# Kernel optimization log

Measured on AMD Instinct MI355X. Metric: run time of the kernel, lower is better.

The kernel has to match this reference:

```python
import jax, jax.numpy as jnp
import numpy as np

N0, N1, N2 = 200000, 100000, 50000
E0, E1 = 1600000, 800000
IN_F, H_F, N_CLS = 128, 256, 64


def sage_conv(h_src, src_idx, dst_idx, num_dst, W_self, W_neigh, b):
    # DGL SAGEConv with aggregator_type='mean':
    #   h_neigh = mean over in-neighbors of h_src
    #   out = h_dst @ W_self + h_neigh @ W_neigh + b
    h_dst = h_src[:num_dst]
    msgs = h_src[src_idx]                                   # [E, F] gather
    summed = jax.ops.segment_sum(msgs, dst_idx, num_segments=num_dst)
    deg = jax.ops.segment_sum(jnp.ones((src_idx.shape[0],), h_src.dtype),
                              dst_idx, num_segments=num_dst)
    h_neigh = summed / jnp.maximum(deg, 1.0)[:, None]       # mean, safe for deg=0
    return h_dst @ W_self + h_neigh @ W_neigh + b


def setup_inputs() -> dict:
    key = jax.random.key(0)
    ks = jax.random.split(key, 10)
    s1 = 1.0 / np.sqrt(IN_F)
    s2 = 1.0 / np.sqrt(H_F)
    return {
        "x": jax.random.normal(ks[0], (N0, IN_F), jnp.float32),
        "src0": jax.random.randint(ks[1], (E0,), 0, N0, jnp.int64 if jax.config.jax_enable_x64 else jnp.int32),
        "dst0": jnp.sort(jax.random.randint(ks[2], (E0,), 0, N1)),
        "src1": jax.random.randint(ks[3], (E1,), 0, N1),
        "dst1": jnp.sort(jax.random.randint(ks[4], (E1,), 0, N2)),
        "num_dst0": N1,
        "num_dst1": N2,
        "W_self1": jax.random.normal(ks[5], (IN_F, H_F), jnp.float32) * s1,
        "W_neigh1": jax.random.normal(ks[6], (IN_F, H_F), jnp.float32) * s1,
        "b1": jnp.zeros((H_F,), jnp.float32),
        "W_self2": jax.random.normal(ks[7], (H_F, N_CLS), jnp.float32) * s2,
        "W_neigh2": jax.random.normal(ks[8], (H_F, N_CLS), jnp.float32) * s2,
        "b2": jnp.zeros((N_CLS,), jnp.float32),
    }


def reference(x, src0, dst0, src1, dst1, num_dst0, num_dst1,
              W_self1, W_neigh1, b1, W_self2, W_neigh2, b2):
    h = sage_conv(x, src0, dst0, num_dst0, W_self1, W_neigh1, b1)   # [N1, H]
    h = jax.nn.relu(h)
    h = sage_conv(h, src1, dst1, num_dst1, W_self2, W_neigh2, b2)   # [N2, C]
    return h
```

## Files before the change

### kernel.cpp

```cpp
#include <hip/hip_runtime.h>

constexpr int cN0  = 200000;
constexpr int cN1  = 100000;
constexpr int cN2  = 50000;
constexpr int cE0  = 1600000;
constexpr int cE1  = 800000;
constexpr int cIN  = 128;
constexpr int cH   = 256;
constexpr int cCLS = 64;

constexpr float QSTEP = 6.0f / 127.0f;
constexpr float QINV  = 127.0f / 6.0f;

using bf16x8 = __attribute__((ext_vector_type(8))) short;
using f32x4  = __attribute__((ext_vector_type(4))) float;

__device__ __forceinline__ float bflo(unsigned int u) {
    union { unsigned int i; float f; } v; v.i = u << 16; return v.f;
}
__device__ __forceinline__ float bfhi(unsigned int u) {
    union { unsigned int i; float f; } v; v.i = u & 0xFFFF0000u; return v.f;
}
__device__ __forceinline__ unsigned int f2bf(float f) {
    union { float f; unsigned int i; } v; v.f = f;
    return (v.i + 0x7FFFu + ((v.i >> 16) & 1u)) >> 16;
}

constexpr int XBLK = (cN0 * cIN / 8) / 256;
constexpr int WCNT = cH * cH + 2 * cCLS * cH;
constexpr int WBLK = WCNT / 256;
constexpr int RCNT = (cN1 + 1) + (cN2 + 1);
constexpr int RBLK = (RCNT + 255) / 256;

__global__ __launch_bounds__(256) void prep(
        const float* __restrict__ x,
        const float* __restrict__ Ws1, const float* __restrict__ Wn1,
        const float* __restrict__ Wn2, const float* __restrict__ Ws2,
        const int* __restrict__ dst0, const int* __restrict__ dst1,
        unsigned short* __restrict__ xb, unsigned int* __restrict__ xq,
        unsigned short* __restrict__ Wt1, unsigned short* __restrict__ Wt2,
        int* __restrict__ row0, int* __restrict__ row1) {
    const int b = blockIdx.x, tid = threadIdx.x;
    if (b < XBLK) {
        const int i = b * 256 + tid;
        const float4* p = (const float4*)x + (size_t)i * 2;
        float4 a = p[0], c = p[1];
        uint4 o;
        o.x = f2bf(a.x) | (f2bf(a.y) << 16);
        o.y = f2bf(a.z) | (f2bf(a.w) << 16);
        o.z = f2bf(c.x) | (f2bf(c.y) << 16);
        o.w = f2bf(c.z) | (f2bf(c.w) << 16);
        ((uint4*)xb)[i] = o;
        auto q8 = [](float v) -> unsigned int {
            int q = __float2int_rn(v * QINV);
            q = q > 127 ? 127 : (q < -127 ? -127 : q);
            return (unsigned int)q & 255u;
        };
        uint2 d;
        d.x = q8(a.x) | (q8(a.y) << 8) | (q8(a.z) << 16) | (q8(a.w) << 24);
        d.y = q8(c.x) | (q8(c.y) << 8) | (q8(c.z) << 16) | (q8(c.w) << 24);
        ((uint2*)xq)[i] = d;
    } else if (b < XBLK + WBLK) {
        const int wi = (b - XBLK) * 256 + tid;
        if (wi < cH * cH) {
            int n = wi >> 8, k = wi & 255;
            float v = (k < cIN) ? Ws1[k * cH + n] : Wn1[(k - cIN) * cH + n];
            Wt1[n * cH + k] = (unsigned short)f2bf(v);
        } else {
            int j = wi - cH * cH; int n = j >> 8, k = j & 255;
            float v = (n < cCLS) ? Wn2[k * cCLS + n] : Ws2[k * cCLS + (n - cCLS)];
            Wt2[n * cH + k] = (unsigned short)f2bf(v);
        }
    } else {
        const int ti = (b - XBLK - WBLK) * 256 + tid;
        if (ti <= cN1) {
            int lo = 0, hi = cE0;
            while (lo < hi) { int mid = (lo + hi) >> 1; if (dst0[mid] < ti) lo = mid + 1; else hi = mid; }
            row0[ti] = lo;
        } else {
            int d = ti - (cN1 + 1);
            if (d <= cN2) {
                int lo = 0, hi = cE1;
                while (lo < hi) { int mid = (lo + hi) >> 1; if (dst1[mid] < d) lo = mid + 1; else hi = mid; }
                row1[d] = lo;
            }
        }
    }
}

__global__ __launch_bounds__(256) void agg_i8(
        const uint2* __restrict__ xq,
        const int* __restrict__ sidx,
        const int* __restrict__ rows,
        unsigned short* __restrict__ nb,
        int num_dst) {
    const int tid = threadIdx.x, lane = tid & 63;
    const int m = blockIdx.x * 4 + (tid >> 6);
    if (m >= num_dst) return;
    const int sub = lane >> 4, t = lane & 15;
    const int e0 = rows[m], e1 = rows[m + 1];

    int acc[8];
    #pragma unroll
    for (int j = 0; j < 8; ++j) acc[j] = 0;
    auto addq = [&](uint2 v) {
        #pragma unroll
        for (int d = 0; d < 2; ++d) {
            unsigned int w = (&v.x)[d];
            acc[d * 4 + 0] += (int)(signed char)(w);
            acc[d * 4 + 1] += (int)(signed char)(w >> 8);
            acc[d * 4 + 2] += (int)(signed char)(w >> 16);
            acc[d * 4 + 3] += (int)(signed char)(w >> 24);
        }
    };

    int base = e0;
    for (; base + 16 <= e1; base += 16) {
        int sA = sidx[base + sub];
        int sB = sidx[base + 4 + sub];
        int sC = sidx[base + 8 + sub];
        int sD = sidx[base + 12 + sub];
        uint2 vA = xq[(size_t)sA * 16 + t];
        uint2 vB = xq[(size_t)sB * 16 + t];
        uint2 vC = xq[(size_t)sC * 16 + t];
        uint2 vD = xq[(size_t)sD * 16 + t];
        addq(vA); addq(vB); addq(vC); addq(vD);
    }
    for (; base < e1; base += 4) {
        int idx = base + sub;
        if (idx < e1) addq(xq[(size_t)sidx[idx] * 16 + t]);
    }

    #pragma unroll
    for (int j = 0; j < 8; ++j) {
        acc[j] += __shfl_xor(acc[j], 16, 64);
        acc[j] += __shfl_xor(acc[j], 32, 64);
    }

    if (sub == 0) {
        const int deg = e1 - e0;
        const float f = QSTEP / (float)(deg > 1 ? deg : 1);
        uint4 w;
        w.x = f2bf(acc[0] * f) | (f2bf(acc[1] * f) << 16);
        w.y = f2bf(acc[2] * f) | (f2bf(acc[3] * f) << 16);
        w.z = f2bf(acc[4] * f) | (f2bf(acc[5] * f) << 16);
        w.w = f2bf(acc[6] * f) | (f2bf(acc[7] * f) << 16);
        ((uint4*)nb)[(size_t)m * 16 + t] = w;
    }
}

template<int K, bool ACCUM>
__global__ __launch_bounds__(256) void agg_wave(
        const unsigned short* __restrict__ src,
        const int* __restrict__ sidx,
        const int* __restrict__ rows,
        void* __restrict__ outv, int num_dst) {
    constexpr int LPR = K / 8;
    constexpr int EPW = 64 / LPR;
    const int tid = threadIdx.x;
    const int lane = tid & 63;
    const int m = blockIdx.x * 4 + (tid >> 6);
    if (m >= num_dst) return;
    const int sub = lane / LPR;
    const int t   = lane % LPR;

    const uint4* s4 = (const uint4*)src;
    const int e0 = rows[m], e1 = rows[m + 1];

    float acc[8];
    #pragma unroll
    for (int j = 0; j < 8; ++j) acc[j] = 0.f;
    auto addv = [&](uint4 v) {
        acc[0] += bflo(v.x); acc[1] += bfhi(v.x);
        acc[2] += bflo(v.y); acc[3] += bfhi(v.y);
        acc[4] += bflo(v.z); acc[5] += bfhi(v.z);
        acc[6] += bflo(v.w); acc[7] += bfhi(v.w);
    };

    int base = e0;
    for (; base + 2 * EPW <= e1; base += 2 * EPW) {
        int sA = sidx[base + sub], sB = sidx[base + EPW + sub];
        uint4 vA = s4[(size_t)sA * LPR + t];
        uint4 vB = s4[(size_t)sB * LPR + t];
        addv(vA); addv(vB);
    }
    for (; base < e1; base += EPW) {
        int idx = base + sub;
        if (idx < e1) addv(s4[(size_t)sidx[idx] * LPR + t]);
    }

    #pragma unroll
    for (int j = 0; j < 8; ++j) {
        #pragma unroll
        for (int off = LPR; off < 64; off <<= 1)
            acc[j] += __shfl_xor(acc[j], off, 64);
    }

    if (sub == 0) {
        const int deg = e1 - e0;
        const float inv = 1.0f / (float)(deg > 1 ? deg : 1);
        if (!ACCUM) {
            uint4 o;
            o.x = f2bf(acc[0] * inv) | (f2bf(acc[1] * inv) << 16);
            o.y = f2bf(acc[2] * inv) | (f2bf(acc[3] * inv) << 16);
            o.z = f2bf(acc[4] * inv) | (f2bf(acc[5] * inv) << 16);
            o.w = f2bf(acc[6] * inv) | (f2bf(acc[7] * inv) << 16);
            ((uint4*)outv)[(size_t)m * LPR + t] = o;
        } else {
            float* op = (float*)outv + (size_t)m * K + t * 8;
            float4 o0 = *(float4*)op, o1 = *(float4*)(op + 4);
            o0.x += acc[0] * inv; o0.y += acc[1] * inv;
            o0.z += acc[2] * inv; o0.w += acc[3] * inv;
            o1.x += acc[4] * inv; o1.y += acc[5] * inv;
            o1.z += acc[6] * inv; o1.w += acc[7] * inv;
            *(float4*)op = o0; *(float4*)(op + 4) = o1;
        }
    }
}

template<int BM, int BN, int WM, int WN, bool RELU, bool HASBIAS, bool OUTBF16>
__global__ __launch_bounds__(256) void gemm_mfma(
        const unsigned short* __restrict__ A1, int K1,
        const unsigned short* __restrict__ A2, int K2,
        const unsigned short* __restrict__ Bt,
        const float* __restrict__ bias,
        void* __restrict__ Cout, int M, int N) {
    static_assert(2 * WM * 16 == BM && 2 * WN * 16 == BN, "wave tiling");
    __shared__ unsigned short As[BM][40];
    __shared__ unsigned short Bs[BN][40];

    const int tid = threadIdx.x;
    const int m0 = blockIdx.x * BM, n0 = blockIdx.y * BN;
    const int lane = tid & 63, wave = tid >> 6;
    const int wrow = wave >> 1, wcol = wave & 1;
    const int quad = lane >> 4, l16 = lane & 15;
    const int K = K1 + K2;

    f32x4 acc[WM][WN];
    #pragma unroll
    for (int i = 0; i < WM; ++i)
        #pragma unroll
        for (int j = 0; j < WN; ++j)
            acc[i][j] = (f32x4){0.f, 0.f, 0.f, 0.f};

    for (int kb = 0; kb < K; kb += 32) {
        const unsigned short* Ab; int lda, kloc;
        if (kb < K1) { Ab = A1; lda = K1; kloc = kb; }
        else         { Ab = A2; lda = K2; kloc = kb - K1; }

        #pragma unroll
        for (int f = 0; f < (BM * 4) / 256; ++f) {
            int idx = tid + f * 256;
            int row = idx >> 2, q = idx & 3;
            int gm = m0 + row;
            uint4 v = make_uint4(0, 0, 0, 0);
            if (gm < M) v = *(const uint4*)(Ab + (size_t)gm * lda + kloc + q * 8);
            *(uint4*)&As[row][q * 8] = v;
        }
        #pragma unroll
        for (int f = 0; f < (BN * 4) / 256; ++f) {
            int idx = tid + f * 256;
            int row = idx >> 2, q = idx & 3;
            uint4 v = *(const uint4*)(Bt + (size_t)(n0 + row) * K + kb + q * 8);
            *(uint4*)&Bs[row][q * 8] = v;
        }
        __syncthreads();

        bf16x8 a[WM], b[WN];
        #pragma unroll
        for (int i = 0; i < WM; ++i)
            a[i] = *(const bf16x8*)&As[(wrow * WM + i) * 16 + l16][quad * 8];
        #pragma unroll
        for (int j = 0; j < WN; ++j)
            b[j] = *(const bf16x8*)&Bs[(wcol * WN + j) * 16 + l16][quad * 8];
        #pragma unroll
        for (int i = 0; i < WM; ++i)
            #pragma unroll
            for (int j = 0; j < WN; ++j)
                acc[i][j] = __builtin_amdgcn_mfma_f32_16x16x32_bf16(
                    a[i], b[j], acc[i][j], 0, 0, 0);
        __syncthreads();
    }

    float bv[WN];
    #pragma unroll
    for (int j = 0; j < WN; ++j)
        bv[j] = HASBIAS ? bias[n0 + (wcol * WN + j) * 16 + l16] : 0.f;
    #pragma unroll
    for (int i = 0; i < WM; ++i) {
        #pragma unroll
        for (int r = 0; r < 4; ++r) {
            int gm = m0 + (wrow * WM + i) * 16 + quad * 4 + r;
            if (gm >= M) continue;
            #pragma unroll
            for (int j = 0; j < WN; ++j) {
                int gn = n0 + (wcol * WN + j) * 16 + l16;
                float v = acc[i][j][r] + bv[j];
                if (RELU) v = fmaxf(v, 0.f);
                if (OUTBF16)
                    ((unsigned short*)Cout)[(size_t)gm * N + gn] = (unsigned short)f2bf(v);
                else
                    ((float*)Cout)[(size_t)gm * N + gn] = v;
            }
        }
    }
}

__global__ __launch_bounds__(256) void gemm2_split(
        const unsigned short* __restrict__ A,
        const unsigned short* __restrict__ Bt,
        const float* __restrict__ b2,
        unsigned short* __restrict__ zb,
        float* __restrict__ out) {
    __shared__ unsigned short As[128][40];
    __shared__ unsigned short Bs[128][40];
    const int tid = threadIdx.x;
    const int m0 = blockIdx.x * 128;
    const int lane = tid & 63, wave = tid >> 6;
    const int wrow = wave >> 1, wcol = wave & 1;
    const int quad = lane >> 4, l16 = lane & 15;

    f32x4 acc[4][4];
    #pragma unroll
    for (int i = 0; i < 4; ++i)
        #pragma unroll
        for (int j = 0; j < 4; ++j)
            acc[i][j] = (f32x4){0.f, 0.f, 0.f, 0.f};

    for (int kb = 0; kb < cH; kb += 32) {
        #pragma unroll
        for (int f = 0; f < 2; ++f) {
            int idx = tid + f * 256;
            int row = idx >> 2, q = idx & 3;
            int gm = m0 + row;
            uint4 v = make_uint4(0, 0, 0, 0);
            if (gm < cN1) v = *(const uint4*)(A + (size_t)gm * cH + kb + q * 8);
            *(uint4*)&As[row][q * 8] = v;
        }
        #pragma unroll
        for (int f = 0; f < 2; ++f) {
            int idx = tid + f * 256;
            int row = idx >> 2, q = idx & 3;
            uint4 v = *(const uint4*)(Bt + (size_t)row * cH + kb + q * 8);
            *(uint4*)&Bs[row][q * 8] = v;
        }
        __syncthreads();

        bf16x8 a[4], b[4];
        #pragma unroll
        for (int i = 0; i < 4; ++i)
            a[i] = *(const bf16x8*)&As[(wrow * 4 + i) * 16 + l16][quad * 8];
        #pragma unroll
        for (int j = 0; j < 4; ++j)
            b[j] = *(const bf16x8*)&Bs[(wcol * 4 + j) * 16 + l16][quad * 8];
        #pragma unroll
        for (int i = 0; i < 4; ++i)
            #pragma unroll
            for (int j = 0; j < 4; ++j)
                acc[i][j] = __builtin_amdgcn_mfma_f32_16x16x32_bf16(
                    a[i], b[j], acc[i][j], 0, 0, 0);
        __syncthreads();
    }

    if (wcol == 0) {
        #pragma unroll
        for (int i = 0; i < 4; ++i) {
            #pragma unroll
            for (int r = 0; r < 4; ++r) {
                int gm = m0 + (wrow * 4 + i) * 16 + quad * 4 + r;
                if (gm >= cN1) continue;
                #pragma unroll
                for (int j = 0; j < 4; ++j) {
                    int gn = j * 16 + l16;
                    zb[(size_t)gm * cCLS + gn] = (unsigned short)f2bf(acc[i][j][r]);
                }
            }
        }
    } else {
        float bv[4];
        #pragma unroll
        for (int j = 0; j < 4; ++j) bv[j] = b2[j * 16 + l16];
        #pragma unroll
        for (int i = 0; i < 4; ++i) {
            #pragma unroll
            for (int r = 0; r < 4; ++r) {
                int gm = m0 + (wrow * 4 + i) * 16 + quad * 4 + r;
                if (gm >= cN2) continue;
                #pragma unroll
                for (int j = 0; j < 4; ++j)
                    out[(size_t)gm * cCLS + j * 16 + l16] = acc[i][j][r] + bv[j];
            }
        }
    }
}

extern "C" void kernel_launch(void* const* d_in, const int* in_sizes, int n_in,
                              void* d_out, int out_size, void* d_ws, size_t ws_size,
                              hipStream_t stream) {
    const float* x      = (const float*)d_in[0];
    const int*   src0   = (const int*)d_in[1];
    const int*   dst0   = (const int*)d_in[2];
    const int*   src1   = (const int*)d_in[3];
    const int*   dst1   = (const int*)d_in[4];
    const float* Wself1  = (const float*)d_in[7];
    const float* Wneigh1 = (const float*)d_in[8];
    const float* b1      = (const float*)d_in[9];
    const float* Wself2  = (const float*)d_in[10];
    const float* Wneigh2 = (const float*)d_in[11];
    const float* b2      = (const float*)d_in[12];
    float* out = (float*)d_out;

    char* ws = (char*)d_ws;
    int* row0 = (int*)ws;
    int* row1 = row0 + (cN1 + 1);
    size_t off = (size_t)((cN1 + 1) + (cN2 + 1)) * sizeof(int);
    off = (off + 1023) & ~(size_t)1023;
    unsigned short* xb = (unsigned short*)(ws + off); off += (size_t)cN0 * cIN * 2;
    unsigned int*   xq = (unsigned int*)(ws + off);
    unsigned short* zb = (unsigned short*)(ws + off); off += (size_t)cN0 * cIN;
    unsigned short* nb  = (unsigned short*)(ws + off); off += (size_t)cN1 * cIN * 2;
    unsigned short* h1b = (unsigned short*)(ws + off); off += (size_t)cN1 * cH * 2;
    unsigned short* Wt1 = (unsigned short*)(ws + off); off += (size_t)cH * cH * 2;
    unsigned short* Wt2 = (unsigned short*)(ws + off); off += (size_t)2 * cCLS * cH * 2;

    prep<<<XBLK + WBLK + RBLK, 256, 0, stream>>>(
        x, Wself1, Wneigh1, Wneigh2, Wself2, dst0, dst1,
        xb, xq, Wt1, Wt2, row0, row1);

    agg_i8<<<(cN1 + 3) / 4, 256, 0, stream>>>(
        (const uint2*)xq, src0, row0, nb, cN1);

    gemm_mfma<128, 128, 4, 4, true, true, true>
        <<<dim3((cN1 + 127) / 128, cH / 128), 256, 0, stream>>>(
        xb, cIN, nb, cIN, Wt1, b1, h1b, cN1, cH);

    gemm2_split<<<(cN1 + 127) / 128, 256, 0, stream>>>(h1b, Wt2, b2, zb, out);

    agg_wave<cCLS, true><<<(cN2 + 3) / 4, 256, 0, stream>>>(
        zb, src1, row1, out, cN2);
}
```

Measured before the change: 341.6 us.

## Pack biased uint8 sums in SWAR accumulators and convert only needed bf16 rows

```diff
diff --git a/kernel.cpp b/kernel.cpp
--- a/kernel.cpp
+++ b/kernel.cpp
@@ -26,7 +26,11 @@
     return (v.i + 0x7FFFu + ((v.i >> 16) & 1u)) >> 16;
 }
 
-constexpr int XBLK = (cN0 * cIN / 8) / 256;
+constexpr int PV   = 8;
+constexpr int AF4  = cN1 * cIN / 4;
+constexpr int ABLK = (AF4 + 256 * PV - 1) / (256 * PV);
+constexpr int BF4  = (cN0 - cN1) * cIN / 4;
+constexpr int BBLK = (BF4 + 256 * PV - 1) / (256 * PV);
 constexpr int WCNT = cH * cH + 2 * cCLS * cH;
 constexpr int WBLK = WCNT / 256;
 constexpr int RCNT = (cN1 + 1) + (cN2 + 1);
@@ -41,27 +45,43 @@
         unsigned short* __restrict__ Wt1, unsigned short* __restrict__ Wt2,
         int* __restrict__ row0, int* __restrict__ row1) {
     const int b = blockIdx.x, tid = threadIdx.x;
-    if (b < XBLK) {
-        const int i = b * 256 + tid;
-        const float4* p = (const float4*)x + (size_t)i * 2;
-        float4 a = p[0], c = p[1];
-        uint4 o;
-        o.x = f2bf(a.x) | (f2bf(a.y) << 16);
-        o.y = f2bf(a.z) | (f2bf(a.w) << 16);
-        o.z = f2bf(c.x) | (f2bf(c.y) << 16);
-        o.w = f2bf(c.z) | (f2bf(c.w) << 16);
-        ((uint4*)xb)[i] = o;
-        auto q8 = [](float v) -> unsigned int {
-            int q = __float2int_rn(v * QINV);
+    if (b < ABLK + BBLK) {
+        const bool hasXB = (b < ABLK);
+        const int  lb    = hasXB ? b : b - ABLK;
+        const int  limit = hasXB ? AF4 : BF4;
+        const int  base  = lb * 256 * PV + tid;
+        const float4* xp = (const float4*)x + (hasXB ? 0 : (size_t)AF4);
+        const int  xqoff = hasXB ? 0 : AF4;
+
+        float4 v[PV];
+        #pragma unroll
+        for (int j = 0; j < PV; ++j) {
+            int idx = base + j * 256;
+            int cidx = idx < limit ? idx : limit - 1;
+            v[j] = xp[cidx];
+        }
+        auto q8b = [](float f) -> unsigned int {
+            int q = __float2int_rn(f * QINV);
             q = q > 127 ? 127 : (q < -127 ? -127 : q);
-            return (unsigned int)q & 255u;
+            return (unsigned int)(q + 128);
         };
-        uint2 d;
-        d.x = q8(a.x) | (q8(a.y) << 8) | (q8(a.z) << 16) | (q8(a.w) << 24);
-        d.y = q8(c.x) | (q8(c.y) << 8) | (q8(c.z) << 16) | (q8(c.w) << 24);
-        ((uint2*)xq)[i] = d;
-    } else if (b < XBLK + WBLK) {
-        const int wi = (b - XBLK) * 256 + tid;
+        #pragma unroll
+        for (int j = 0; j < PV; ++j) {
+            int idx = base + j * 256;
+            if (idx >= limit) continue;
+            float4 a = v[j];
+            if (hasXB) {
+                uint2 o;
+                o.x = f2bf(a.x) | (f2bf(a.y) << 16);
+                o.y = f2bf(a.z) | (f2bf(a.w) << 16);
+                ((uint2*)xb)[idx] = o;
+            }
+            unsigned int d = q8b(a.x) | (q8b(a.y) << 8) |
+                             (q8b(a.z) << 16) | (q8b(a.w) << 24);
+            xq[xqoff + idx] = d;
+        }
+    } else if (b < ABLK + BBLK + WBLK) {
+        const int wi = (b - ABLK - BBLK) * 256 + tid;
         if (wi < cH * cH) {
             int n = wi >> 8, k = wi & 255;
             float v = (k < cIN) ? Ws1[k * cH + n] : Wn1[(k - cIN) * cH + n];
@@ -72,7 +92,7 @@
             Wt2[n * cH + k] = (unsigned short)f2bf(v);
         }
     } else {
-        const int ti = (b - XBLK - WBLK) * 256 + tid;
+        const int ti = (b - ABLK - BBLK - WBLK) * 256 + tid;
         if (ti <= cN1) {
             int lo = 0, hi = cE0;
             while (lo < hi) { int mid = (lo + hi) >> 1; if (dst0[mid] < ti) lo = mid + 1; else hi = mid; }
@@ -100,18 +120,12 @@
     const int sub = lane >> 4, t = lane & 15;
     const int e0 = rows[m], e1 = rows[m + 1];
 
-    int acc[8];
-    #pragma unroll
-    for (int j = 0; j < 8; ++j) acc[j] = 0;
+    unsigned int accA = 0, accB = 0, accC = 0, accD = 0;
     auto addq = [&](uint2 v) {
-        #pragma unroll
-        for (int d = 0; d < 2; ++d) {
-            unsigned int w = (&v.x)[d];
-            acc[d * 4 + 0] += (int)(signed char)(w);
-            acc[d * 4 + 1] += (int)(signed char)(w >> 8);
-            acc[d * 4 + 2] += (int)(signed char)(w >> 16);
-            acc[d * 4 + 3] += (int)(signed char)(w >> 24);
-        }
+        accA += v.x & 0x00FF00FFu;
+        accB += (v.x >> 8) & 0x00FF00FFu;
+        accC += v.y & 0x00FF00FFu;
+        accD += (v.y >> 8) & 0x00FF00FFu;
     };
 
     int base = e0;
@@ -131,20 +145,27 @@
         if (idx < e1) addq(xq[(size_t)sidx[idx] * 16 + t]);
     }
 
-    #pragma unroll
-    for (int j = 0; j < 8; ++j) {
-        acc[j] += __shfl_xor(acc[j], 16, 64);
-        acc[j] += __shfl_xor(acc[j], 32, 64);
-    }
+    accA += __shfl_xor((int)accA, 16, 64); accA += __shfl_xor((int)accA, 32, 64);
+    accB += __shfl_xor((int)accB, 16, 64); accB += __shfl_xor((int)accB, 32, 64);
+    accC += __shfl_xor((int)accC, 16, 64); accC += __shfl_xor((int)accC, 32, 64);
+    accD += __shfl_xor((int)accD, 16, 64); accD += __shfl_xor((int)accD, 32, 64);
 
     if (sub == 0) {
         const int deg = e1 - e0;
-        const float f = QSTEP / (float)(deg > 1 ? deg : 1);
+        const float inv  = QSTEP / (float)(deg > 1 ? deg : 1);
+        const float bias = 128.0f * (float)deg;
+        auto cv = [&](unsigned int field) -> float {
+            return ((float)(int)field - bias) * inv;
+        };
+        float f0 = cv(accA & 0xFFFFu), f2 = cv(accA >> 16);
+        float f1 = cv(accB & 0xFFFFu), f3 = cv(accB >> 16);
+        float f4 = cv(accC & 0xFFFFu), f6 = cv(accC >> 16);
+        float f5 = cv(accD & 0xFFFFu), f7 = cv(accD >> 16);
         uint4 w;
-        w.x = f2bf(acc[0] * f) | (f2bf(acc[1] * f) << 16);
-        w.y = f2bf(acc[2] * f) | (f2bf(acc[3] * f) << 16);
-        w.z = f2bf(acc[4] * f) | (f2bf(acc[5] * f) << 16);
-        w.w = f2bf(acc[6] * f) | (f2bf(acc[7] * f) << 16);
+        w.x = f2bf(f0) | (f2bf(f1) << 16);
+        w.y = f2bf(f2) | (f2bf(f3) << 16);
+        w.z = f2bf(f4) | (f2bf(f5) << 16);
+        w.w = f2bf(f6) | (f2bf(f7) << 16);
         ((uint4*)nb)[(size_t)m * 16 + t] = w;
     }
 }
@@ -415,7 +436,7 @@
     int* row1 = row0 + (cN1 + 1);
     size_t off = (size_t)((cN1 + 1) + (cN2 + 1)) * sizeof(int);
     off = (off + 1023) & ~(size_t)1023;
-    unsigned short* xb = (unsigned short*)(ws + off); off += (size_t)cN0 * cIN * 2;
+    unsigned short* xb = (unsigned short*)(ws + off); off += (size_t)cN1 * cIN * 2;
     unsigned int*   xq = (unsigned int*)(ws + off);
     unsigned short* zb = (unsigned short*)(ws + off); off += (size_t)cN0 * cIN;
     unsigned short* nb  = (unsigned short*)(ws + off); off += (size_t)cN1 * cIN * 2;
@@ -423,7 +444,7 @@
     unsigned short* Wt1 = (unsigned short*)(ws + off); off += (size_t)cH * cH * 2;
     unsigned short* Wt2 = (unsigned short*)(ws + off); off += (size_t)2 * cCLS * cH * 2;
 
-    prep<<<XBLK + WBLK + RBLK, 256, 0, stream>>>(
+    prep<<<ABLK + BBLK + WBLK + RBLK, 256, 0, stream>>>(
         x, Wself1, Wneigh1, Wneigh2, Wself2, dst0, dst1,
         xb, xq, Wt1, Wt2, row0, row1);
 
```

Result: no change. 335.0 us (-2.0%).
